# Kernel optimization log

Measured on AMD Instinct MI355X. Metric: run time of the kernel, lower is better.

Reference implementation:

```python
import jax, jax.numpy as jnp
import numpy as np

H, D, VD = 8, 64, 64
QD, KD, VDIM, OUT = 512, 512, 512, 512
N, QS, VS = 16, 512, 512
TEMP = 10.0              # softstair_temp
SCALING = D ** -0.5


def _softstair(x):
    fl = jnp.floor(x)
    return fl + jax.nn.sigmoid(TEMP * (jnp.abs(x - fl) - 0.5))


def setup_inputs() -> dict:
    key = jax.random.key(0)
    ks = jax.random.split(key, 24)
    f = jax.random.normal
    s = 0.03  # xavier-ish scale
    return {
        "Q": f(ks[0], (N, QS, QD), jnp.float32),
        "K": f(ks[1], (N, VS, KD), jnp.float32),
        "V": f(ks[2], (N, VS, VDIM), jnp.float32),
        "past_state": f(ks[3], (N, H, QS, D), jnp.float32),
        "past_attention": jax.random.uniform(ks[4], (N, H, QS, 1), jnp.float32),
        "value_positions": jnp.arange(VS, dtype=jnp.float32),
        "attention_mask": jnp.ones((N, QS, VS), jnp.int32),
        "Wq": f(ks[5], (QD, H * D), jnp.float32) * s,
        "Wk": f(ks[6], (KD, H * D), jnp.float32) * s,
        "Wv": f(ks[7], (VDIM, H * VD), jnp.float32) * s,
        "Wpos": f(ks[8], (QD, H * D), jnp.float32) * s,
        "bpos": f(ks[9], (H * D,), jnp.float32) * s,
        "Wsigma": f(ks[10], (H, D, 1), jnp.float32) * s,
        "Wrho": f(ks[11], (H, D, 3), jnp.float32) * s,
        "mix_w": f(ks[12], (QD, 1), jnp.float32) * s,
        "mix_b": f(ks[13], (1,), jnp.float32) * s,
        "gru_wi": f(ks[14], (D, 3 * D), jnp.float32) * s,
        "gru_wh": f(ks[15], (D, 3 * D), jnp.float32) * s,
        "gru_bi": f(ks[16], (3 * D,), jnp.float32) * s,
        "gru_bh": f(ks[17], (3 * D,), jnp.float32) * s,
        "Wc": f(ks[18], (H * VD, OUT), jnp.float32) * s,
    }


def reference(Q, K, V, past_state, past_attention, value_positions, attention_mask,
              Wq, Wk, Wv, Wpos, bpos, Wsigma, Wrho, mix_w, mix_b,
              gru_wi, gru_wh, gru_bi, gru_bh, Wc):
    n, qS, _ = Q.shape
    vS = K.shape[1]
    mask_f = attention_mask.astype(jnp.float32)          # [N,qS,vS]
    mask_b = attention_mask.astype(bool)[:, None]        # [N,1,qS,vS]
    lengths = jnp.sum(mask_f, axis=-1)                   # [N,qS]
    l_1 = jnp.maximum(1.0, lengths - 1.0)[:, None, :, None]
    step_size = 1.0 / l_1                                # [N,1,qS,1]
    nvp = value_positions[None, None, None, :] * step_size  # [N,1,qS,vS]

    # mix gate
    mix = jax.nn.sigmoid(Q @ mix_w + mix_b)[:, None]     # [N,1,qS,1]

    # projections -> [N,H,S,d]
    Qpos = (Q @ Wpos + bpos).reshape(n, qS, H, D).transpose(0, 2, 1, 3)
    Qh = (Q @ Wq).reshape(n, qS, H, D).transpose(0, 2, 1, 3)
    Kh = (K @ Wk).reshape(n, vS, H, D).transpose(0, 2, 1, 3)
    Vh = (V @ Wv).reshape(n, vS, H, VD).transpose(0, 2, 1, 3)

    # content attention
    content = jnp.einsum('bhqd,bhkd->bhqk', Qh, Kh) * SCALING
    content_attn = jax.nn.softmax(jnp.where(mask_b, content, -jnp.inf), axis=-1)

    # GRUCell update (torch gate order r,z,n) on relu(Qpos) with past_state
    x = jax.nn.relu(Qpos)
    gi = x @ gru_wi + gru_bi
    gh = past_state @ gru_wh + gru_bh
    ir, iz, inn = jnp.split(gi, 3, axis=-1)
    hr, hz, hn = jnp.split(gh, 3, axis=-1)
    r = jax.nn.sigmoid(ir + hr)
    z = jax.nn.sigmoid(iz + hz)
    nn_ = jnp.tanh(inn + r * hn)
    state = (1.0 - z) * nn_ + z * past_state             # [N,H,qS,D]

    # location (Gaussian) attention
    sigma = (jax.nn.relu(jnp.einsum('bhqd,hde->bhqe', state, Wsigma)) + 0.27) \
            / lengths[:, None, :, None]                  # [N,H,qS,1]
    rho = jnp.einsum('bhqd,hde->bhqe', state, Wrho)      # [N,H,qS,3]
    steps = _softstair(rho[..., 0:1])
    attn_gate = jax.nn.sigmoid(rho[..., 1:2])
    bias_gate = jax.nn.sigmoid(rho[..., 2:3])
    mu_ = steps * step_size + attn_gate * past_attention + bias_gate
    # leaky clamp to [0,1]
    mu = jnp.maximum(0.01 * mu_, jnp.minimum(mu_, 1.0 + 0.01 * mu_))
    diff = nvp - mu                                      # [N,H,qS,vS]
    gauss = jnp.exp(-(diff * diff) / (2.0 * sigma * sigma))
    g = gauss * mask_f[:, None]
    pos_attn = g / jnp.sum(g + 1e-20, axis=-1, keepdims=True)

    scores = mix * pos_attn + (1.0 - mix) * content_attn
    attended = jnp.einsum('bhqk,bhkv->bhqv', scores, Vh)
    out = attended.transpose(0, 2, 1, 3).reshape(n, qS, H * VD) @ Wc
    return out
```

## Files before the change

kernel.cpp:

```cpp
#include <hip/hip_runtime.h>


typedef __bf16 bf16;
typedef __bf16 bfx8 __attribute__((ext_vector_type(8)));
typedef float v4f __attribute__((ext_vector_type(4)));

__device__ inline float sigm(float x) { return 1.0f / (1.0f + __expf(-x)); }
__device__ inline float tanh_fast(float x) { return 1.0f - 2.0f / (__expf(2.0f * x) + 1.0f); }

__device__ inline v4f mfma16(bfx8 a, bfx8 b, v4f c) {
    return __builtin_amdgcn_mfma_f32_16x16x32_bf16(a, b, c, 0, 0, 0);
}

typedef const __attribute__((address_space(1))) void* gvp;
typedef __attribute__((address_space(3))) void* lvp;

__device__ inline void gload_lds16(const bf16* g, bf16* l) {
    __builtin_amdgcn_global_load_lds((gvp)g, (lvp)l, 16, 0, 0);
}

__device__ inline void split8(const float* __restrict__ p, bfx8& hi, bfx8& lo) {
    float4 x = *(const float4*)p;
    float4 y = *(const float4*)(p + 4);
    float v[8] = {x.x, x.y, x.z, x.w, y.x, y.y, y.z, y.w};
#pragma unroll
    for (int j = 0; j < 8; ++j) {
        bf16 h = (bf16)v[j];
        hi[j] = h;
        lo[j] = (bf16)(v[j] - (float)h);
    }
}

struct TW { const float* src[5]; bf16* dst[5]; bf16* dstlo[5]; };

__global__ __launch_bounds__(256) void trans_w_kernel(TW a) {
    __shared__ float tile[64][68];
    const float* src = a.src[blockIdx.y];
    bf16* dst = a.dst[blockIdx.y];
    bf16* dlo = a.dstlo[blockIdx.y];
    const int rbase = (blockIdx.x >> 3) * 64, cbase = (blockIdx.x & 7) * 64;
    const int t = threadIdx.x;
    const int r = t >> 2, cc = (t & 3) * 16;
    {
        const float* p = src + (long)(rbase + r) * 512 + cbase + cc;
        *(float4*)(&tile[r][cc]) = *(const float4*)p;
        *(float4*)(&tile[r][cc + 4]) = *(const float4*)(p + 4);
        *(float4*)(&tile[r][cc + 8]) = *(const float4*)(p + 8);
        *(float4*)(&tile[r][cc + 12]) = *(const float4*)(p + 12);
    }
    __syncthreads();
    {
        bfx8 h0, h1, l0, l1;
#pragma unroll
        for (int j = 0; j < 8; ++j) {
            float v0 = tile[cc + j][r];
            float v1 = tile[cc + 8 + j][r];
            bf16 a0 = (bf16)v0, a1 = (bf16)v1;
            h0[j] = a0; l0[j] = (bf16)(v0 - (float)a0);
            h1[j] = a1; l1[j] = (bf16)(v1 - (float)a1);
        }
        const int n_ = cbase + r;
        const int x_ = (n_ & 7) << 3;
        const long rowo = (long)n_ * 512;
        const int ka = (rbase + cc) ^ x_;
        const int kb = (rbase + cc + 8) ^ x_;
        *(bfx8*)(dst + rowo + ka) = h0;
        *(bfx8*)(dst + rowo + kb) = h1;
        if (dlo) {
            *(bfx8*)(dlo + rowo + ka) = l0;
            *(bfx8*)(dlo + rowo + kb) = l1;
        }
    }
}

__global__ void gru_prep_kernel(const float* __restrict__ gwi, const float* __restrict__ gwh,
                                bf16* ih, bf16* il, bf16* hh, bf16* hl) {
    const float* src = blockIdx.x ? gwh : gwi;
    bf16* dh = blockIdx.x ? hh : ih;
    bf16* dl = blockIdx.x ? hl : il;
    int n = threadIdx.x;
    for (int k = 0; k < 64; ++k) {
        float v = src[k * 192 + n];
        bf16 h = (bf16)v;
        dh[n * 64 + k] = h;
        dl[n * 64 + k] = (bf16)(v - (float)h);
    }
}

struct GEMMDesc {
    const float* Af;
    const bf16* Ab;
    const bf16* B0;
    const bf16* B1;
    const float* bias;
    bf16* Cb;
    bf16* Cl;
    float* Cf;
    int mode;
};
struct G4 { GEMMDesc d[4]; };

__global__ __launch_bounds__(256, 2) void gemm128(G4 gg) {
    __shared__ bf16 sm[32768];

    const GEMMDesc g = gg.d[blockIdx.z];
    const int mode = g.mode;
    const int mbase = blockIdx.x * 128, nbase = blockIdx.y * 128;
    const int t = threadIdx.x, w = t >> 6, l = t & 63;
    const int quad = l >> 4, c = l & 15;
    const int wr = w >> 1, wc = w & 1;

    const v4f zero4 = {0.f, 0.f, 0.f, 0.f};
    v4f acc[4][4];
#pragma unroll
    for (int m = 0; m < 4; ++m)
#pragma unroll
        for (int nn = 0; nn < 4; ++nn) acc[m][nn] = zero4;

    const int nsteps = (mode == 2) ? 24 : 8;
    const int arow_t = t >> 3;
    const int ach = t & 7;
    const int asw = ((ach ^ (arow_t & 7)) * 8);
    const int xm = c & 7;
    const int slot0 = w * 4;
    const int srow = l >> 3;
    const int sch8 = (l & 7) * 8;

    float4 ax[4], ay[4];

    auto issue = [&](int s, bf16* As, bf16* Bs) {
        const bf16* Bsrc = g.B0;
        int k0;
        if (mode == 2) {
            int ph = s >> 3;
            k0 = (s & 7) * 64;
            if (ph == 1) Bsrc = g.B1;
        } else {
            k0 = s * 64;
        }
#pragma unroll
        for (int j = 0; j < 4; ++j) {
            int sl = slot0 + j;
            int row = sl * 8 + srow;
            gload_lds16(Bsrc + (long)(nbase + row) * 512 + k0 + sch8, Bs + sl * 512);
        }
        if (mode == 3) {
#pragma unroll
            for (int j = 0; j < 4; ++j) {
                int sl = slot0 + j;
                int row = sl * 8 + srow;
                gload_lds16(g.Ab + (long)(mbase + row) * 512 + k0 + sch8, As + sl * 512);
            }
        } else {
#pragma unroll
            for (int j = 0; j < 4; ++j) {
                const float* p = g.Af + (long)(mbase + j * 32 + arow_t) * 512 + k0 + ach * 8;
                ax[j] = *(const float4*)p;
                ay[j] = *(const float4*)(p + 4);
            }
        }
    };

    auto writeA = [&](int s, bf16* As) {
        if (mode == 3) return;
        const bool lo = (mode == 2) && ((s >> 3) == 2);
#pragma unroll
        for (int j = 0; j < 4; ++j) {
            float v[8] = {ax[j].x, ax[j].y, ax[j].z, ax[j].w,
                          ay[j].x, ay[j].y, ay[j].z, ay[j].w};
            bfx8 hv;
            if (!lo) {
#pragma unroll
                for (int q = 0; q < 8; ++q) hv[q] = (bf16)v[q];
            } else {
#pragma unroll
                for (int q = 0; q < 8; ++q) {
                    bf16 h = (bf16)v[q];
                    hv[q] = (bf16)(v[q] - (float)h);
                }
            }
            *(bfx8*)(&As[(j * 32 + arow_t) * 64 + asw]) = hv;
        }
    };

    auto compute = [&](const bf16* As, const bf16* Bs) {
#pragma unroll
        for (int ks = 0; ks < 2; ++ks) {
            const int off = (((ks * 4 + quad) ^ xm) * 8);
            bfx8 af[4], bb[4];
#pragma unroll
            for (int m = 0; m < 4; ++m)
                af[m] = *(const bfx8*)(&As[(wr * 64 + m * 16 + c) * 64 + off]);
#pragma unroll
            for (int nn = 0; nn < 4; ++nn)
                bb[nn] = *(const bfx8*)(&Bs[(wc * 64 + nn * 16 + c) * 64 + off]);
#pragma unroll
            for (int m = 0; m < 4; ++m)
#pragma unroll
                for (int nn = 0; nn < 4; ++nn)
                    acc[m][nn] = mfma16(af[m], bb[nn], acc[m][nn]);
        }
    };

    issue(0, sm, sm + 8192);
    writeA(0, sm);
    __syncthreads();
    for (int s = 0; s < nsteps; ++s) {
        bf16* Ac = sm + (s & 1) * 16384;
        bf16* An = sm + (((s & 1) ^ 1) * 16384);
        const bool more = (s + 1 < nsteps);
        if (more) issue(s + 1, An, An + 8192);
        compute(Ac, Ac + 8192);
        if (more) writeA(s + 1, An);
        __syncthreads();
    }

    if (mode == 3) {
        float* C = g.Cf;
#pragma unroll
        for (int m = 0; m < 4; ++m)
#pragma unroll
            for (int nn = 0; nn < 4; ++nn)
#pragma unroll
                for (int i = 0; i < 4; ++i) {
                    int row = mbase + wr * 64 + m * 16 + quad * 4 + i;
                    int col = nbase + wc * 64 + nn * 16 + c;
                    C[(long)row * 512 + col] = acc[m][nn][i];
                }
        return;
    }

    if (mode == 1) {
        bf16* CT = g.Cb + ((long)(mbase >> 9)) * 262144;
        const int s0 = mbase & 511;
        for (int h = 0; h < 2; ++h) {
            if (wr == h) {
#pragma unroll
                for (int m = 0; m < 4; ++m)
#pragma unroll
                    for (int nn = 0; nn < 4; ++nn)
#pragma unroll
                        for (int i = 0; i < 4; ++i)
                            sm[(wc * 64 + nn * 16 + c) * 64 + m * 16 + quad * 4 + i] =
                                (bf16)acc[m][nn][i];
            }
            __syncthreads();
            {
                const bf16* src = sm + (t >> 1) * 64 + (t & 1) * 32;
                bf16* d = CT + (long)(nbase + (t >> 1)) * 512 + s0 + h * 64 + (t & 1) * 32;
#pragma unroll
                for (int j = 0; j < 4; ++j) *(bfx8*)(d + j * 8) = *(const bfx8*)(src + j * 8);
            }
            __syncthreads();
        }
        return;
    }

    for (int h = 0; h < 2; ++h) {
        if (wr == h) {
#pragma unroll
            for (int m = 0; m < 4; ++m)
#pragma unroll
                for (int nn = 0; nn < 4; ++nn)
#pragma unroll
                    for (int i = 0; i < 4; ++i) {
                        int col = wc * 64 + nn * 16 + c;
                        float v = acc[m][nn][i];
                        if (mode == 2) v = fmaxf(v + g.bias[nbase + col], 0.f);
                        bf16 hv = (bf16)v;
                        sm[(m * 16 + quad * 4 + i) * 128 + col] = hv;
                        if (mode == 2)
                            sm[8192 + (m * 16 + quad * 4 + i) * 128 + col] =
                                (bf16)(v - (float)hv);
                    }
        }
        __syncthreads();
        {
            const int row = t >> 2, seg = t & 3;
            const bf16* src = sm + row * 128 + seg * 32;
            bf16* d = g.Cb + (long)(mbase + h * 64 + row) * 512 + nbase + seg * 32;
#pragma unroll
            for (int j = 0; j < 4; ++j) *(bfx8*)(d + j * 8) = *(const bfx8*)(src + j * 8);
            if (mode == 2) {
                const bf16* src2 = sm + 8192 + row * 128 + seg * 32;
                bf16* d2 = g.Cl + (long)(mbase + h * 64 + row) * 512 + nbase + seg * 32;
#pragma unroll
                for (int j = 0; j < 4; ++j) *(bfx8*)(d2 + j * 8) = *(const bfx8*)(src2 + j * 8);
            }
        }
        __syncthreads();
    }
}

__global__ __launch_bounds__(256) void mix_len_kernel(
    const float* __restrict__ Q, const int* __restrict__ mask,
    const float* __restrict__ mix_w, const float* __restrict__ mix_b,
    float* __restrict__ mixv, float* __restrict__ stepv, float* __restrict__ lenv,
    unsigned* __restrict__ maskbits) {
    int row = blockIdx.x * 4 + (threadIdx.x >> 6);
    int lane = threadIdx.x & 63;
    float dot = 0.f, ms = 0.f;
    unsigned myw = 0;
#pragma unroll
    for (int j = 0; j < 8; ++j) {
        float qv = Q[(long)row * 512 + j * 64 + lane];
        float wv = mix_w[j * 64 + lane];
        dot += qv * wv;
        int mv = mask[(long)row * 512 + j * 64 + lane];
        unsigned long long b = __ballot(mv != 0);
        ms += (float)__popcll(b);
        if ((lane >> 1) == j) myw = (unsigned)(b >> ((lane & 1) * 32));
    }
#pragma unroll
    for (int o = 32; o > 0; o >>= 1) dot += __shfl_xor(dot, o);
    if (lane < 16) maskbits[(long)row * 16 + lane] = myw;
    if (lane == 0) {
        mixv[row] = sigm(dot + mix_b[0]);
        lenv[row] = ms;
        stepv[row] = 1.0f / fmaxf(1.0f, ms - 1.0f);
    }
}

__global__ __launch_bounds__(256) void gru_fused_kernel(
    const bf16* __restrict__ Xh, const bf16* __restrict__ Xl,
    const float* __restrict__ hp,
    const bf16* __restrict__ wih, const bf16* __restrict__ wil,
    const bf16* __restrict__ whh, const bf16* __restrict__ whl,
    const float* __restrict__ gbi, const float* __restrict__ gbh,
    const float* __restrict__ pa, const float* __restrict__ Wsigma,
    const float* __restrict__ Wrho,
    const float* __restrict__ lenv, const float* __restrict__ stepv,
    float* __restrict__ muv, float* __restrict__ sigv) {
    __shared__ bf16 Wh[192][72], Wl[192][72];
    __shared__ float biL[384];

    const int b = blockIdx.x;
    const int qb = b & 7, nh = b >> 3, hd = nh & 7, n = nh >> 3;
    const int t = threadIdx.x;
    const int w = t >> 6, lane = t & 63, quad = lane >> 4, c = lane & 15;
    const int q0 = qb * 64 + w * 16;

    if (t < 192) { biL[t] = gbi[t]; biL[192 + t] = gbh[t]; }
#pragma unroll
    for (int it = 0; it < 6; ++it) {
        int task = it * 256 + t;
        int r = task >> 3, ch = task & 7;
        *(bfx8*)(&Wh[r][ch * 8]) = *(const bfx8*)(wih + r * 64 + ch * 8);
        *(bfx8*)(&Wl[r][ch * 8]) = *(const bfx8*)(wil + r * 64 + ch * 8);
    }
    __syncthreads();

    const v4f zero4 = {0.f, 0.f, 0.f, 0.f};
    v4f gi[12], gh[12];
#pragma unroll
    for (int nt = 0; nt < 12; ++nt) gi[nt] = zero4;
#pragma unroll
    for (int ks = 0; ks < 2; ++ks) {
        long ao = (long)(n * 512 + q0 + c) * 512 + hd * 64 + ks * 32 + quad * 8;
        bfx8 xh = *(const bfx8*)(Xh + ao);
        bfx8 xl = *(const bfx8*)(Xl + ao);
#pragma unroll
        for (int nt = 0; nt < 12; ++nt) {
            bfx8 bh = *(const bfx8*)(&Wh[nt * 16 + c][ks * 32 + quad * 8]);
            bfx8 bl = *(const bfx8*)(&Wl[nt * 16 + c][ks * 32 + quad * 8]);
            gi[nt] = mfma16(xh, bh, gi[nt]);
            gi[nt] = mfma16(xh, bl, gi[nt]);
            gi[nt] = mfma16(xl, bh, gi[nt]);
        }
    }
    __syncthreads();
#pragma unroll
    for (int it = 0; it < 6; ++it) {
        int task = it * 256 + t;
        int r = task >> 3, ch = task & 7;
        *(bfx8*)(&Wh[r][ch * 8]) = *(const bfx8*)(whh + r * 64 + ch * 8);
        *(bfx8*)(&Wl[r][ch * 8]) = *(const bfx8*)(whl + r * 64 + ch * 8);
    }
    __syncthreads();
#pragma unroll
    for (int nt = 0; nt < 12; ++nt) gh[nt] = zero4;
#pragma unroll
    for (int ks = 0; ks < 2; ++ks) {
        bfx8 ah, al;
        split8(hp + (long)(nh * 512 + q0 + c) * 64 + ks * 32 + quad * 8, ah, al);
#pragma unroll
        for (int nt = 0; nt < 12; ++nt) {
            bfx8 bh = *(const bfx8*)(&Wh[nt * 16 + c][ks * 32 + quad * 8]);
            bfx8 bl = *(const bfx8*)(&Wl[nt * 16 + c][ks * 32 + quad * 8]);
            gh[nt] = mfma16(ah, bh, gh[nt]);
            gh[nt] = mfma16(ah, bl, gh[nt]);
            gh[nt] = mfma16(al, bh, gh[nt]);
        }
    }

    float st[4][4];
#pragma unroll
    for (int t4 = 0; t4 < 4; ++t4) {
        float bir = biL[t4 * 16 + c];
        float biz = biL[64 + t4 * 16 + c];
        float bin = biL[128 + t4 * 16 + c];
        float bhr = biL[192 + t4 * 16 + c];
        float bhz = biL[256 + t4 * 16 + c];
        float bhn = biL[320 + t4 * 16 + c];
#pragma unroll
        for (int i = 0; i < 4; ++i) {
            int row = q0 + quad * 4 + i;
            float r = sigm(gi[t4][i] + bir + gh[t4][i] + bhr);
            float z = sigm(gi[t4 + 4][i] + biz + gh[t4 + 4][i] + bhz);
            float nn_ = tanh_fast(gi[t4 + 8][i] + bin + r * (gh[t4 + 8][i] + bhn));
            float hpv = hp[(long)(nh * 512 + row) * 64 + t4 * 16 + c];
            st[t4][i] = (1.0f - z) * nn_ + z * hpv;
        }
    }

    float ws_[4], wr0[4], wr1[4], wr2[4];
#pragma unroll
    for (int t4 = 0; t4 < 4; ++t4) {
        int d = t4 * 16 + c;
        ws_[t4] = Wsigma[hd * 64 + d];
        wr0[t4] = Wrho[(hd * 64 + d) * 3 + 0];
        wr1[t4] = Wrho[(hd * 64 + d) * 3 + 1];
        wr2[t4] = Wrho[(hd * 64 + d) * 3 + 2];
    }
#pragma unroll
    for (int i = 0; i < 4; ++i) {
        float s0 = 0.f, s1 = 0.f, s2 = 0.f, s3 = 0.f;
#pragma unroll
        for (int t4 = 0; t4 < 4; ++t4) {
            float sv = st[t4][i];
            s0 += sv * ws_[t4];
            s1 += sv * wr0[t4];
            s2 += sv * wr1[t4];
            s3 += sv * wr2[t4];
        }
#pragma unroll
        for (int o = 1; o < 16; o <<= 1) {
            s0 += __shfl_xor(s0, o);
            s1 += __shfl_xor(s1, o);
            s2 += __shfl_xor(s2, o);
            s3 += __shfl_xor(s3, o);
        }
        if (c == 0) {
            int row = q0 + quad * 4 + i;
            int idx = nh * 512 + row, rq = n * 512 + row;
            float L = lenv[rq], sp = stepv[rq];
            float sg = (fmaxf(s0, 0.f) + 0.27f) / L;
            float fl = floorf(s1);
            float steps = fl + sigm(10.0f * (fabsf(s1 - fl) - 0.5f));
            float ag = sigm(s2), bg = sigm(s3);
            float mu_ = steps * sp + ag * pa[idx] + bg;
            float mu = fmaxf(0.01f * mu_, fminf(mu_, 1.0f + 0.01f * mu_));
            muv[idx] = mu;
            sigv[idx] = sg;
        }
    }
}

__global__ __launch_bounds__(256) void attn_fused_kernel(
    const bf16* __restrict__ Qh, const bf16* __restrict__ Kh,
    const bf16* __restrict__ VhT, const unsigned* __restrict__ maskbits,
    const float* __restrict__ vpos, const float* __restrict__ mixv,
    const float* __restrict__ stepv, const float* __restrict__ muv,
    const float* __restrict__ sigv, bf16* __restrict__ att) {
    __shared__ bf16 Pp[16][520];
    __shared__ bf16 Pg[16][520];
    __shared__ float rsum[4][16], rgsum[4][16];

    const int b = blockIdx.x;
    const int nh = ((b >> 8) << 3) | (b & 7);
    const int qt = (b >> 3) & 31;
    const int hd = nh & 7, n = nh >> 3;
    const int t = threadIdx.x;
    const int wave = t >> 6, lane = t & 63;
    const int quad = lane >> 4, c = lane & 15;
    const int qloc = quad * 4;

    const bf16* qrow = Qh + (long)(n * 512 + qt * 16 + c) * 512 + hd * 64 + quad * 8;
    bfx8 afr0 = *(const bfx8*)qrow;
    bfx8 afr1 = *(const bfx8*)(qrow + 32);

    const v4f zero4 = {0.f, 0.f, 0.f, 0.f};
    v4f acc[8];
#pragma unroll
    for (int i = 0; i < 8; ++i) acc[i] = zero4;

    const bf16* kbase = Kh + (long)(n * 512 + wave * 128 + c) * 512 + hd * 64 + quad * 8;
#pragma unroll
    for (int t8 = 0; t8 < 8; ++t8) {
        bfx8 b0 = *(const bfx8*)(kbase + (long)t8 * 16 * 512);
        bfx8 b1 = *(const bfx8*)(kbase + (long)t8 * 16 * 512 + 32);
        acc[t8] = mfma16(afr0, b0, acc[t8]);
        acc[t8] = mfma16(afr1, b1, acc[t8]);
    }

    float mu_[4], i2s[4], stp[4];
#pragma unroll
    for (int i = 0; i < 4; ++i) {
        int q = qt * 16 + qloc + i;
        int idx = nh * 512 + q, rq = n * 512 + q;
        mu_[i] = muv[idx];
        float sg = sigv[idx];
        i2s[i] = 0.5f / (sg * sg);
        stp[i] = stepv[rq];
    }

    unsigned mbits[4];
    {
        const unsigned* mrow = maskbits + ((long)(n * 512 + qt * 16) << 4) + wave * 4;
#pragma unroll
        for (int i = 0; i < 4; ++i) {
            const unsigned* mr = mrow + ((qloc + i) << 4);
            unsigned w0 = mr[0], w1 = mr[1], w2 = mr[2], w3 = mr[3];
            mbits[i] = ((w0 >> c) & 1u) | (((w0 >> (16 + c)) & 1u) << 1) |
                       (((w1 >> c) & 1u) << 2) | (((w1 >> (16 + c)) & 1u) << 3) |
                       (((w2 >> c) & 1u) << 4) | (((w2 >> (16 + c)) & 1u) << 5) |
                       (((w3 >> c) & 1u) << 6) | (((w3 >> (16 + c)) & 1u) << 7);
        }
    }

    float vp[8];
#pragma unroll
    for (int t8 = 0; t8 < 8; ++t8) vp[t8] = vpos[wave * 128 + t8 * 16 + c];

    float psum[4] = {0.f, 0.f, 0.f, 0.f};
    float gsum[4] = {0.f, 0.f, 0.f, 0.f};
#pragma unroll
    for (int i = 0; i < 4; ++i) {
        float m = mu_[i], s = stp[i], c2 = i2s[i];
#pragma unroll
        for (int t8 = 0; t8 < 8; ++t8) {
            int on = (mbits[i] >> t8) & 1;
            float pv = on ? __expf(acc[t8][i] * 0.125f) : 0.f;
            float d = vp[t8] * s - m;
            float gv = on ? __expf(-(d * d) * c2) : 0.f;
            psum[i] += pv;
            gsum[i] += gv;
            int k = wave * 128 + t8 * 16 + c;
            Pp[qloc + i][k] = (bf16)pv;
            Pg[qloc + i][k] = (bf16)gv;
        }
    }
#pragma unroll
    for (int i = 0; i < 4; ++i) {
#pragma unroll
        for (int o = 1; o < 16; o <<= 1) {
            psum[i] += __shfl_xor(psum[i], o);
            gsum[i] += __shfl_xor(gsum[i], o);
        }
        if (c == 0) {
            rsum[wave][qloc + i] = psum[i];
            rgsum[wave][qloc + i] = gsum[i];
        }
    }

    __syncthreads();

    float ac[4], bc[4];
#pragma unroll
    for (int i = 0; i < 4; ++i) {
        float Sp = rsum[0][qloc + i] + rsum[1][qloc + i] + rsum[2][qloc + i] + rsum[3][qloc + i];
        float Sg = rgsum[0][qloc + i] + rgsum[1][qloc + i] + rgsum[2][qloc + i] +
                   rgsum[3][qloc + i] + 512.0f * 1e-20f;
        float m_ = mixv[n * 512 + qt * 16 + qloc + i];
        ac[i] = (1.0f - m_) / Sp;
        bc[i] = m_ / Sg;
    }

    v4f accP = zero4, accG = zero4;
    const bf16* vrow = VhT + (long)(n * 512 + hd * 64 + wave * 16 + c) * 512 + quad * 8;
#pragma unroll
    for (int ks = 0; ks < 16; ++ks) {
        bfx8 bf_ = *(const bfx8*)(vrow + ks * 32);
        bfx8 ap = *(const bfx8*)(&Pp[c][ks * 32 + quad * 8]);
        bfx8 ag = *(const bfx8*)(&Pg[c][ks * 32 + quad * 8]);
        accP = mfma16(ap, bf_, accP);
        accG = mfma16(ag, bf_, accG);
    }

#pragma unroll
    for (int i = 0; i < 4; ++i) {
        int q = qt * 16 + quad * 4 + i;
        int cx = (wave * 16 + c) ^ (((quad * 4 + i) & 7) << 3);
        att[(long)(n * 512 + q) * 512 + hd * 64 + cx] =
            (bf16)(ac[i] * accP[i] + bc[i] * accG[i]);
    }
}

extern "C" void kernel_launch(void* const* d_in, const int* in_sizes, int n_in,
                              void* d_out, int out_size, void* d_ws, size_t ws_size,
                              hipStream_t stream) {
    (void)in_sizes; (void)n_in; (void)out_size; (void)ws_size;

    const float* Q = (const float*)d_in[0];
    const float* K = (const float*)d_in[1];
    const float* V = (const float*)d_in[2];
    const float* past_state = (const float*)d_in[3];
    const float* past_att = (const float*)d_in[4];
    const float* vpos = (const float*)d_in[5];
    const int* mask = (const int*)d_in[6];
    const float* Wq = (const float*)d_in[7];
    const float* Wk = (const float*)d_in[8];
    const float* Wv = (const float*)d_in[9];
    const float* Wpos = (const float*)d_in[10];
    const float* bpos = (const float*)d_in[11];
    const float* Wsigma = (const float*)d_in[12];
    const float* Wrho = (const float*)d_in[13];
    const float* mix_w = (const float*)d_in[14];
    const float* mix_b = (const float*)d_in[15];
    const float* gwi = (const float*)d_in[16];
    const float* gwh = (const float*)d_in[17];
    const float* gbi = (const float*)d_in[18];
    const float* gbh = (const float*)d_in[19];
    const float* Wc = (const float*)d_in[20];
    float* out = (float*)d_out;

    char* p = (char*)d_ws;
    const size_t SZB = 8192UL * 512 * 2;
    const size_t SZW = 512UL * 512 * 2;
    bf16* WqT = (bf16*)p;   p += SZW;
    bf16* WkT = (bf16*)p;   p += SZW;
    bf16* WvT = (bf16*)p;   p += SZW;
    bf16* WpT = (bf16*)p;   p += SZW;
    bf16* WpTl = (bf16*)p;  p += SZW;
    bf16* WcT = (bf16*)p;   p += SZW;
    bf16* wih = (bf16*)p;   p += 24576;
    bf16* wil = (bf16*)p;   p += 24576;
    bf16* whh = (bf16*)p;   p += 24576;
    bf16* whl = (bf16*)p;   p += 24576;
    bf16* Qh = (bf16*)p;    p += SZB;
    bf16* Kh = (bf16*)p;    p += SZB;
    bf16* VhT = (bf16*)p;   p += SZB;
    bf16* Xh = (bf16*)p;
    bf16* att = Xh;         p += SZB;
    bf16* Xl = (bf16*)p;    p += SZB;
    unsigned* maskbits = (unsigned*)p;   p += 8192UL * 16 * 4;
    float* mixv = (float*)p;  p += 32768;
    float* stepv = (float*)p; p += 32768;
    float* lenv = (float*)p;  p += 32768;
    float* muv = (float*)p;   p += 262144;
    float* sigv = (float*)p;  p += 262144;

    dim3 blk(256);

    TW tw;
    tw.src[0] = Wq; tw.src[1] = Wk; tw.src[2] = Wv; tw.src[3] = Wpos; tw.src[4] = Wc;
    tw.dst[0] = WqT; tw.dst[1] = WkT; tw.dst[2] = WvT; tw.dst[3] = WpT; tw.dst[4] = WcT;
    tw.dstlo[0] = nullptr; tw.dstlo[1] = nullptr; tw.dstlo[2] = nullptr;
    tw.dstlo[3] = WpTl; tw.dstlo[4] = nullptr;
    trans_w_kernel<<<dim3(64, 5), blk, 0, stream>>>(tw);

    gru_prep_kernel<<<dim3(2), dim3(192), 0, stream>>>(gwi, gwh, wih, wil, whh, whl);

    mix_len_kernel<<<dim3(2048), blk, 0, stream>>>(Q, mask, mix_w, mix_b, mixv, stepv, lenv, maskbits);

    G4 gp;
    gp.d[0].Af = Q;  gp.d[0].Ab = nullptr; gp.d[0].B0 = WpT; gp.d[0].B1 = WpTl;
    gp.d[0].bias = bpos; gp.d[0].Cb = Xh; gp.d[0].Cl = Xl; gp.d[0].Cf = nullptr; gp.d[0].mode = 2;
    gp.d[1].Af = Q;  gp.d[1].Ab = nullptr; gp.d[1].B0 = WqT; gp.d[1].B1 = nullptr;
    gp.d[1].bias = nullptr; gp.d[1].Cb = Qh; gp.d[1].Cl = nullptr; gp.d[1].Cf = nullptr; gp.d[1].mode = 0;
    gp.d[2].Af = K;  gp.d[2].Ab = nullptr; gp.d[2].B0 = WkT; gp.d[2].B1 = nullptr;
    gp.d[2].bias = nullptr; gp.d[2].Cb = Kh; gp.d[2].Cl = nullptr; gp.d[2].Cf = nullptr; gp.d[2].mode = 0;
    gp.d[3].Af = V;  gp.d[3].Ab = nullptr; gp.d[3].B0 = WvT; gp.d[3].B1 = nullptr;
    gp.d[3].bias = nullptr; gp.d[3].Cb = VhT; gp.d[3].Cl = nullptr; gp.d[3].Cf = nullptr; gp.d[3].mode = 1;
    gemm128<<<dim3(64, 4, 4), blk, 0, stream>>>(gp);

    gru_fused_kernel<<<dim3(1024), blk, 0, stream>>>(
        Xh, Xl, past_state, wih, wil, whh, whl, gbi, gbh, past_att, Wsigma, Wrho,
        lenv, stepv, muv, sigv);

    attn_fused_kernel<<<dim3(4096), blk, 0, stream>>>(
        Qh, Kh, VhT, maskbits, vpos, mixv, stepv, muv, sigv, att);

    G4 go;
    go.d[0].Af = nullptr; go.d[0].Ab = att; go.d[0].B0 = WcT; go.d[0].B1 = nullptr;
    go.d[0].bias = nullptr; go.d[0].Cb = nullptr; go.d[0].Cl = nullptr; go.d[0].Cf = out;
    go.d[0].mode = 3;
    go.d[1] = go.d[0]; go.d[2] = go.d[0]; go.d[3] = go.d[0];
    gemm128<<<dim3(64, 4, 1), blk, 0, stream>>>(go);
}
```

Before: 338.1 us.

## Merge prep kernels, pre-swizzle GRU weights and pre-pack mask bits

```diff
diff --git a/kernel.cpp b/kernel.cpp
--- a/kernel.cpp
+++ b/kernel.cpp
@@ -31,25 +31,35 @@
     }
 }
 
-struct TW { const float* src[5]; bf16* dst[5]; bf16* dstlo[5]; };
-
-__global__ __launch_bounds__(256) void trans_w_kernel(TW a) {
-    __shared__ float tile[64][68];
-    const float* src = a.src[blockIdx.y];
-    bf16* dst = a.dst[blockIdx.y];
-    bf16* dlo = a.dstlo[blockIdx.y];
-    const int rbase = (blockIdx.x >> 3) * 64, cbase = (blockIdx.x & 7) * 64;
+struct PrepArgs {
+    const float* wsrc[5]; bf16* wdst[5]; bf16* wdstlo[5];
+    const float* gwi; const float* gwh;
+    bf16* wih; bf16* wil; bf16* whh; bf16* whl;
+    const float* Q; const int* mask; const float* mix_w; const float* mix_b;
+    float* mixv; float* stepv; float* lenv; unsigned* mpack;
+};
+
+__global__ __launch_bounds__(256) void prep_kernel(PrepArgs a) {
+    __shared__ __align__(16) char smraw[17408];
+    const int b = blockIdx.x;
     const int t = threadIdx.x;
-    const int r = t >> 2, cc = (t & 3) * 16;
-    {
-        const float* p = src + (long)(rbase + r) * 512 + cbase + cc;
-        *(float4*)(&tile[r][cc]) = *(const float4*)p;
-        *(float4*)(&tile[r][cc + 4]) = *(const float4*)(p + 4);
-        *(float4*)(&tile[r][cc + 8]) = *(const float4*)(p + 8);
-        *(float4*)(&tile[r][cc + 12]) = *(const float4*)(p + 12);
-    }
-    __syncthreads();
-    {
+
+    if (b < 320) {
+        float (*tile)[68] = (float(*)[68])smraw;
+        const int wy = b >> 6, bx = b & 63;
+        const float* src = a.wsrc[wy];
+        bf16* dst = a.wdst[wy];
+        bf16* dlo = a.wdstlo[wy];
+        const int rbase = (bx >> 3) * 64, cbase = (bx & 7) * 64;
+        const int r = t >> 2, cc = (t & 3) * 16;
+        {
+            const float* p = src + (long)(rbase + r) * 512 + cbase + cc;
+            *(float4*)(&tile[r][cc]) = *(const float4*)p;
+            *(float4*)(&tile[r][cc + 4]) = *(const float4*)(p + 4);
+            *(float4*)(&tile[r][cc + 8]) = *(const float4*)(p + 8);
+            *(float4*)(&tile[r][cc + 12]) = *(const float4*)(p + 12);
+        }
+        __syncthreads();
         bfx8 h0, h1, l0, l1;
 #pragma unroll
         for (int j = 0; j < 8; ++j) {
@@ -70,20 +80,74 @@
             *(bfx8*)(dlo + rowo + ka) = l0;
             *(bfx8*)(dlo + rowo + kb) = l1;
         }
-    }
-}
-
-__global__ void gru_prep_kernel(const float* __restrict__ gwi, const float* __restrict__ gwh,
-                                bf16* ih, bf16* il, bf16* hh, bf16* hl) {
-    const float* src = blockIdx.x ? gwh : gwi;
-    bf16* dh = blockIdx.x ? hh : ih;
-    bf16* dl = blockIdx.x ? hl : il;
-    int n = threadIdx.x;
-    for (int k = 0; k < 64; ++k) {
-        float v = src[k * 192 + n];
-        bf16 h = (bf16)v;
-        dh[n * 64 + k] = h;
-        dl[n * 64 + k] = (bf16)(v - (float)h);
+        return;
+    }
+
+    if (b < 322) {
+        const int m = b - 320;
+        const float* src = m ? a.gwh : a.gwi;
+        bf16* dh = m ? a.whh : a.wih;
+        bf16* dl = m ? a.whl : a.wil;
+        for (int e = t; e < 12288; e += 256) {
+            int row = e >> 7, col = e & 127;
+            int cc = col >> 3, j = col & 7;
+            int nt = row >> 3, ks = (row >> 2) & 1, quad = row & 3;
+            int k = ks * 32 + quad * 8 + j;
+            float v = src[k * 192 + nt * 16 + cc];
+            bf16 h = (bf16)v;
+            dh[e] = h;
+            dl[e] = (bf16)(v - (float)h);
+        }
+        return;
+    }
+
+    unsigned (*mwords)[16] = (unsigned(*)[16])smraw;
+    const int bm = b - 322;
+    const int qt = bm & 31, n = bm >> 5;
+    const int wave = t >> 6, lane = t & 63;
+#pragma unroll
+    for (int rr = 0; rr < 4; ++rr) {
+        const int rloc = wave * 4 + rr;
+        const long row = (long)n * 512 + qt * 16 + rloc;
+        float dot = 0.f, ms = 0.f;
+        unsigned myw = 0;
+#pragma unroll
+        for (int j = 0; j < 8; ++j) {
+            float qv = a.Q[row * 512 + j * 64 + lane];
+            float wv = a.mix_w[j * 64 + lane];
+            dot += qv * wv;
+            int mv = a.mask[row * 512 + j * 64 + lane];
+            unsigned long long bl = __ballot(mv != 0);
+            ms += (float)__popcll(bl);
+            if ((lane >> 1) == j) myw = (unsigned)(bl >> ((lane & 1) * 32));
+        }
+#pragma unroll
+        for (int o = 32; o > 0; o >>= 1) dot += __shfl_xor(dot, o);
+        if (lane < 16) mwords[rloc][lane] = myw;
+        if (lane == 0) {
+            a.mixv[row] = sigm(dot + a.mix_b[0]);
+            a.lenv[row] = ms;
+            a.stepv[row] = 1.0f / fmaxf(1.0f, ms - 1.0f);
+        }
+    }
+    __syncthreads();
+    {
+        const int quad = (lane >> 4), c = lane & 15;
+        unsigned out = 0;
+#pragma unroll
+        for (int i = 0; i < 4; ++i) {
+            const int rl = quad * 4 + i;
+            unsigned w0 = mwords[rl][wave * 4 + 0];
+            unsigned w1 = mwords[rl][wave * 4 + 1];
+            unsigned w2 = mwords[rl][wave * 4 + 2];
+            unsigned w3 = mwords[rl][wave * 4 + 3];
+            unsigned byte_ = ((w0 >> c) & 1u) | (((w0 >> (16 + c)) & 1u) << 1) |
+                             (((w1 >> c) & 1u) << 2) | (((w1 >> (16 + c)) & 1u) << 3) |
+                             (((w2 >> c) & 1u) << 4) | (((w2 >> (16 + c)) & 1u) << 5) |
+                             (((w3 >> c) & 1u) << 6) | (((w3 >> (16 + c)) & 1u) << 7);
+            out |= byte_ << (8 * i);
+        }
+        a.mpack[(long)bm * 256 + t] = out;
     }
 }
 
@@ -292,35 +356,6 @@
     }
 }
 
-__global__ __launch_bounds__(256) void mix_len_kernel(
-    const float* __restrict__ Q, const int* __restrict__ mask,
-    const float* __restrict__ mix_w, const float* __restrict__ mix_b,
-    float* __restrict__ mixv, float* __restrict__ stepv, float* __restrict__ lenv,
-    unsigned* __restrict__ maskbits) {
-    int row = blockIdx.x * 4 + (threadIdx.x >> 6);
-    int lane = threadIdx.x & 63;
-    float dot = 0.f, ms = 0.f;
-    unsigned myw = 0;
-#pragma unroll
-    for (int j = 0; j < 8; ++j) {
-        float qv = Q[(long)row * 512 + j * 64 + lane];
-        float wv = mix_w[j * 64 + lane];
-        dot += qv * wv;
-        int mv = mask[(long)row * 512 + j * 64 + lane];
-        unsigned long long b = __ballot(mv != 0);
-        ms += (float)__popcll(b);
-        if ((lane >> 1) == j) myw = (unsigned)(b >> ((lane & 1) * 32));
-    }
-#pragma unroll
-    for (int o = 32; o > 0; o >>= 1) dot += __shfl_xor(dot, o);
-    if (lane < 16) maskbits[(long)row * 16 + lane] = myw;
-    if (lane == 0) {
-        mixv[row] = sigm(dot + mix_b[0]);
-        lenv[row] = ms;
-        stepv[row] = 1.0f / fmaxf(1.0f, ms - 1.0f);
-    }
-}
-
 __global__ __launch_bounds__(256) void gru_fused_kernel(
     const bf16* __restrict__ Xh, const bf16* __restrict__ Xl,
     const float* __restrict__ hp,
@@ -331,24 +366,12 @@
     const float* __restrict__ Wrho,
     const float* __restrict__ lenv, const float* __restrict__ stepv,
     float* __restrict__ muv, float* __restrict__ sigv) {
-    __shared__ bf16 Wh[192][72], Wl[192][72];
-    __shared__ float biL[384];
-
     const int b = blockIdx.x;
     const int qb = b & 7, nh = b >> 3, hd = nh & 7, n = nh >> 3;
     const int t = threadIdx.x;
     const int w = t >> 6, lane = t & 63, quad = lane >> 4, c = lane & 15;
     const int q0 = qb * 64 + w * 16;
-
-    if (t < 192) { biL[t] = gbi[t]; biL[192 + t] = gbh[t]; }
-#pragma unroll
-    for (int it = 0; it < 6; ++it) {
-        int task = it * 256 + t;
-        int r = task >> 3, ch = task & 7;
-        *(bfx8*)(&Wh[r][ch * 8]) = *(const bfx8*)(wih + r * 64 + ch * 8);
-        *(bfx8*)(&Wl[r][ch * 8]) = *(const bfx8*)(wil + r * 64 + ch * 8);
-    }
-    __syncthreads();
+    const int fbase = quad * 128 + c * 8;
 
     const v4f zero4 = {0.f, 0.f, 0.f, 0.f};
     v4f gi[12], gh[12];
@@ -361,22 +384,14 @@
         bfx8 xl = *(const bfx8*)(Xl + ao);
 #pragma unroll
         for (int nt = 0; nt < 12; ++nt) {
-            bfx8 bh = *(const bfx8*)(&Wh[nt * 16 + c][ks * 32 + quad * 8]);
-            bfx8 bl = *(const bfx8*)(&Wl[nt * 16 + c][ks * 32 + quad * 8]);
+            const int fo = (nt * 2 + ks) * 512 + fbase;
+            bfx8 bh = *(const bfx8*)(wih + fo);
+            bfx8 bl = *(const bfx8*)(wil + fo);
             gi[nt] = mfma16(xh, bh, gi[nt]);
             gi[nt] = mfma16(xh, bl, gi[nt]);
             gi[nt] = mfma16(xl, bh, gi[nt]);
         }
     }
-    __syncthreads();
-#pragma unroll
-    for (int it = 0; it < 6; ++it) {
-        int task = it * 256 + t;
-        int r = task >> 3, ch = task & 7;
-        *(bfx8*)(&Wh[r][ch * 8]) = *(const bfx8*)(whh + r * 64 + ch * 8);
-        *(bfx8*)(&Wl[r][ch * 8]) = *(const bfx8*)(whl + r * 64 + ch * 8);
-    }
-    __syncthreads();
 #pragma unroll
     for (int nt = 0; nt < 12; ++nt) gh[nt] = zero4;
 #pragma unroll
@@ -385,8 +400,9 @@
         split8(hp + (long)(nh * 512 + q0 + c) * 64 + ks * 32 + quad * 8, ah, al);
 #pragma unroll
         for (int nt = 0; nt < 12; ++nt) {
-            bfx8 bh = *(const bfx8*)(&Wh[nt * 16 + c][ks * 32 + quad * 8]);
-            bfx8 bl = *(const bfx8*)(&Wl[nt * 16 + c][ks * 32 + quad * 8]);
+            const int fo = (nt * 2 + ks) * 512 + fbase;
+            bfx8 bh = *(const bfx8*)(whh + fo);
+            bfx8 bl = *(const bfx8*)(whl + fo);
             gh[nt] = mfma16(ah, bh, gh[nt]);
             gh[nt] = mfma16(ah, bl, gh[nt]);
             gh[nt] = mfma16(al, bh, gh[nt]);
@@ -396,12 +412,12 @@
     float st[4][4];
 #pragma unroll
     for (int t4 = 0; t4 < 4; ++t4) {
-        float bir = biL[t4 * 16 + c];
-        float biz = biL[64 + t4 * 16 + c];
-        float bin = biL[128 + t4 * 16 + c];
-        float bhr = biL[192 + t4 * 16 + c];
-        float bhz = biL[256 + t4 * 16 + c];
-        float bhn = biL[320 + t4 * 16 + c];
+        float bir = gbi[t4 * 16 + c];
+        float biz = gbi[64 + t4 * 16 + c];
+        float bin = gbi[128 + t4 * 16 + c];
+        float bhr = gbh[t4 * 16 + c];
+        float bhz = gbh[64 + t4 * 16 + c];
+        float bhn = gbh[128 + t4 * 16 + c];
 #pragma unroll
         for (int i = 0; i < 4; ++i) {
             int row = q0 + quad * 4 + i;
@@ -458,7 +474,7 @@
 
 __global__ __launch_bounds__(256) void attn_fused_kernel(
     const bf16* __restrict__ Qh, const bf16* __restrict__ Kh,
-    const bf16* __restrict__ VhT, const unsigned* __restrict__ maskbits,
+    const bf16* __restrict__ VhT, const unsigned* __restrict__ mpack,
     const float* __restrict__ vpos, const float* __restrict__ mixv,
     const float* __restrict__ stepv, const float* __restrict__ muv,
     const float* __restrict__ sigv, bf16* __restrict__ att) {
@@ -504,19 +520,10 @@
         stp[i] = stepv[rq];
     }
 
+    const unsigned mb32 = mpack[(long)(n * 32 + qt) * 256 + t];
     unsigned mbits[4];
-    {
-        const unsigned* mrow = maskbits + ((long)(n * 512 + qt * 16) << 4) + wave * 4;
-#pragma unroll
-        for (int i = 0; i < 4; ++i) {
-            const unsigned* mr = mrow + ((qloc + i) << 4);
-            unsigned w0 = mr[0], w1 = mr[1], w2 = mr[2], w3 = mr[3];
-            mbits[i] = ((w0 >> c) & 1u) | (((w0 >> (16 + c)) & 1u) << 1) |
-                       (((w1 >> c) & 1u) << 2) | (((w1 >> (16 + c)) & 1u) << 3) |
-                       (((w2 >> c) & 1u) << 4) | (((w2 >> (16 + c)) & 1u) << 5) |
-                       (((w3 >> c) & 1u) << 6) | (((w3 >> (16 + c)) & 1u) << 7);
-        }
-    }
+#pragma unroll
+    for (int i = 0; i < 4; ++i) mbits[i] = (mb32 >> (8 * i)) & 0xffu;
 
     float vp[8];
 #pragma unroll
@@ -633,7 +640,7 @@
     bf16* Xh = (bf16*)p;
     bf16* att = Xh;         p += SZB;
     bf16* Xl = (bf16*)p;    p += SZB;
-    unsigned* maskbits = (unsigned*)p;   p += 8192UL * 16 * 4;
+    unsigned* mpack = (unsigned*)p;      p += 16UL * 32 * 256 * 4;
     float* mixv = (float*)p;  p += 32768;
     float* stepv = (float*)p; p += 32768;
     float* lenv = (float*)p;  p += 32768;
@@ -642,16 +649,16 @@
 
     dim3 blk(256);
 
-    TW tw;
-    tw.src[0] = Wq; tw.src[1] = Wk; tw.src[2] = Wv; tw.src[3] = Wpos; tw.src[4] = Wc;
-    tw.dst[0] = WqT; tw.dst[1] = WkT; tw.dst[2] = WvT; tw.dst[3] = WpT; tw.dst[4] = WcT;
-    tw.dstlo[0] = nullptr; tw.dstlo[1] = nullptr; tw.dstlo[2] = nullptr;
-    tw.dstlo[3] = WpTl; tw.dstlo[4] = nullptr;
-    trans_w_kernel<<<dim3(64, 5), blk, 0, stream>>>(tw);
-
-    gru_prep_kernel<<<dim3(2), dim3(192), 0, stream>>>(gwi, gwh, wih, wil, whh, whl);
-
-    mix_len_kernel<<<dim3(2048), blk, 0, stream>>>(Q, mask, mix_w, mix_b, mixv, stepv, lenv, maskbits);
+    PrepArgs pa;
+    pa.wsrc[0] = Wq; pa.wsrc[1] = Wk; pa.wsrc[2] = Wv; pa.wsrc[3] = Wpos; pa.wsrc[4] = Wc;
+    pa.wdst[0] = WqT; pa.wdst[1] = WkT; pa.wdst[2] = WvT; pa.wdst[3] = WpT; pa.wdst[4] = WcT;
+    pa.wdstlo[0] = nullptr; pa.wdstlo[1] = nullptr; pa.wdstlo[2] = nullptr;
+    pa.wdstlo[3] = WpTl; pa.wdstlo[4] = nullptr;
+    pa.gwi = gwi; pa.gwh = gwh;
+    pa.wih = wih; pa.wil = wil; pa.whh = whh; pa.whl = whl;
+    pa.Q = Q; pa.mask = mask; pa.mix_w = mix_w; pa.mix_b = mix_b;
+    pa.mixv = mixv; pa.stepv = stepv; pa.lenv = lenv; pa.mpack = mpack;
+    prep_kernel<<<dim3(834), blk, 0, stream>>>(pa);
 
     G4 gp;
     gp.d[0].Af = Q;  gp.d[0].Ab = nullptr; gp.d[0].B0 = WpT; gp.d[0].B1 = WpTl;
@@ -669,7 +676,7 @@
         lenv, stepv, muv, sigv);
 
     attn_fused_kernel<<<dim3(4096), blk, 0, stream>>>(
-        Qh, Kh, VhT, maskbits, vpos, mixv, stepv, muv, sigv, att);
+        Qh, Kh, VhT, mpack, vpos, mixv, stepv, muv, sigv, att);
 
     G4 go;
     go.d[0].Af = nullptr; go.d[0].Ab = att; go.d[0].B0 = WcT; go.d[0].B1 = nullptr;
```

New measurement: 345.5 us. 2.2% more time.
